# Kernel optimization log

Hardware: AMD Instinct MI355X
Metric: run time of the kernel (lower is better)

## Reference

```python
import jax, jax.numpy as jnp
import numpy as np

B, CIN, COUT, H, W = 8, 256, 256, 64, 64


def setup_inputs() -> dict:
    key = jax.random.key(0)
    k1, k2, k3 = jax.random.split(key, 3)
    x = jax.random.normal(k1, (B, CIN, H, W), dtype=jnp.float32)
    style = jax.random.normal(k2, (B, CIN), dtype=jnp.float32)
    # kaiming_normal_ (fan_in = CIN*3*3, gain = sqrt(2))
    fan_in = CIN * 9
    weight = jax.random.normal(k3, (COUT, CIN, 3, 3), dtype=jnp.float32) * np.sqrt(2.0 / fan_in)
    return {"x": x, "style": style, "weight": weight}


def reference(x, style, weight):
    b, cin, h, w = x.shape
    cout = weight.shape[0]
    # modulate: [B, Cout, Cin, 3, 3]
    mw = style[:, None, :, None, None] * weight[None]
    # demodulate
    sigma = jnp.sqrt(jnp.sum(mw * mw, axis=(2, 3, 4), keepdims=True) + 1e-8)
    dw = mw / sigma
    # per-sample conv via grouped convolution (groups = B)
    x_g = x.reshape(1, b * cin, h, w)
    w_g = dw.reshape(b * cout, cin, 3, 3)
    out = jax.lax.conv_general_dilated(
        x_g, w_g,
        window_strides=(1, 1),
        padding=((1, 1), (1, 1)),
        feature_group_count=b,
        dimension_numbers=("NCHW", "OIHW", "NCHW"),
    )
    return out.reshape(b, cout, h, w)
```

## Files before the change

kernel.cpp:

```cpp
#include <hip/hip_runtime.h>

#define B_ 8
#define CIN_ 256
#define COUT_ 256

typedef short short8_t __attribute__((ext_vector_type(8)));
typedef float float16_t __attribute__((ext_vector_type(16)));

#define DWA_SHORTS   (B_ * 9 * 32 * COUT_ * 8)
#define XPRE_SHORTS  (B_ * 8 * 66 * 66 * 32)

__device__ __forceinline__ unsigned short f2bf(float f) {
    union { float f; unsigned u; } v; v.f = f;
    unsigned u = v.u;
    unsigned r = (u + 0x7fffu + ((u >> 16) & 1u)) >> 16;
    return (unsigned short)r;
}

__global__ __launch_bounds__(256) void k_prep(const float* __restrict__ x,
                                              const float* __restrict__ style,
                                              const float* __restrict__ weight,
                                              unsigned short* __restrict__ xpre,
                                              unsigned short* __restrict__ dwA) {
    __shared__ float wlds[4 * 2304];
    const int bid = blockIdx.x;
    const int t = threadIdx.x;

    if (bid < 4224) {
        const int h_out = bid % 66;
        const int t2 = bid / 66;
        const int cb = t2 & 7, b = t2 >> 3;
        const int h_in = h_out - 1;
        unsigned short* dst_row = xpre + ((size_t)(b * 8 + cb) * 66 + h_out) * 66 * 32;
#pragma unroll
        for (int pass = 0; pass < 2; ++pass) {
            int p = t + pass * 256;
            if (p >= 264) break;
            int w_out = p >> 2, g = p & 3;
            int w_in = w_out - 1;
            short8_t v = (short8_t){0, 0, 0, 0, 0, 0, 0, 0};
            if ((unsigned)h_in < 64u && (unsigned)w_in < 64u) {
                const float* xp =
                    x + (((size_t)(b * CIN_ + cb * 32 + g * 8)) * 64 + h_in) * 64 + w_in;
#pragma unroll
                for (int j = 0; j < 8; ++j) v[j] = (short)f2bf(xp[(size_t)j * 4096]);
            }
            *(short8_t*)(dst_row + (size_t)w_out * 32 + g * 8) = v;
        }
    } else {
        const int co0 = (bid - 4224) * 4;
        const int co_l = t >> 6;
        const int lane = t & 63;
        const int co = co0 + co_l;

        const float* wp = weight + (size_t)co0 * 2304;
#pragma unroll
        for (int k = 0; k < 36; ++k) wlds[t + 256 * k] = wp[t + 256 * k];
        __syncthreads();

        float wv[4][9];
        float ss[4];
#pragma unroll
        for (int k = 0; k < 4; ++k) {
            float a = 0.f;
#pragma unroll
            for (int tap = 0; tap < 9; ++tap) {
                float w = wlds[co_l * 2304 + (lane + 64 * k) * 9 + tap];
                wv[k][tap] = w;
                a += w * w;
            }
            ss[k] = a;
        }
        float sv[8][4];
#pragma unroll
        for (int b = 0; b < 8; ++b)
#pragma unroll
            for (int k = 0; k < 4; ++k) sv[b][k] = style[b * CIN_ + lane + 64 * k];

        float inv[8];
#pragma unroll
        for (int b = 0; b < 8; ++b) {
            float part = 0.f;
#pragma unroll
            for (int k = 0; k < 4; ++k) part += sv[b][k] * sv[b][k] * ss[k];
#pragma unroll
            for (int off = 32; off > 0; off >>= 1) part += __shfl_xor(part, off, 64);
            inv[b] = 1.0f / sqrtf(part + 1e-8f);
        }

        const size_t base = (size_t)co * 8 + (lane & 7) + (size_t)(lane >> 3) * 2048;
#pragma unroll
        for (int b = 0; b < 8; ++b)
#pragma unroll
            for (int tap = 0; tap < 9; ++tap)
#pragma unroll
                for (int k = 0; k < 4; ++k) {
                    size_t addr = ((size_t)(b * 9 + tap) * 32 + k * 8) * 2048 + base;
                    dwA[addr] = f2bf(wv[k][tap] * sv[b][k] * inv[b]);
                }
    }
}

__global__ __launch_bounds__(256, 4) void k_conv(const unsigned short* __restrict__ xpre,
                                                 const unsigned short* __restrict__ dwA,
                                                 float* __restrict__ out) {
    __shared__ __align__(16) unsigned short xs[2][12 * 66 * 8];

    const int row = blockIdx.x;
    const int co_tile = blockIdx.y;
    const int b = blockIdx.z;
    const int tid = threadIdx.x;
    const int lane = tid & 63, wid = tid >> 6;
    const int wave_m = wid >> 1, wave_n = wid & 1;
    const int l32 = lane & 31, kh = lane >> 5;
    const int co_base = co_tile * 128 + wave_m * 64;

    float16_t acc[2];
#pragma unroll
    for (int mi = 0; mi < 2; ++mi)
#pragma unroll
        for (int r = 0; r < 16; ++r) acc[mi][r] = 0.f;

    short8_t st[4];
    auto load_regs = [&](int cb) {
        const unsigned short* s = xpre + (((size_t)(b * 8 + cb) * 66 + row)) * (66 * 32);
#pragma unroll
        for (int it = 0; it < 3; ++it) {
            int c = tid + it * 256;
            int rowg = c / 66;
            int col = c - rowg * 66;
            st[it] = *(const short8_t*)(s + (size_t)((rowg >> 2) * 2112 + col * 32 + (rowg & 3) * 8));
        }
        if (tid < 24) {
            int c = tid + 768;
            int rowg = c / 66;
            int col = c - rowg * 66;
            st[3] = *(const short8_t*)(s + (size_t)((rowg >> 2) * 2112 + col * 32 + (rowg & 3) * 8));
        }
    };
    auto store_lds = [&](int buf) {
        unsigned short* d = xs[buf];
#pragma unroll
        for (int it = 0; it < 3; ++it)
            *(short8_t*)(d + (size_t)(tid + it * 256) * 8) = st[it];
        if (tid < 24) *(short8_t*)(d + (size_t)(tid + 768) * 8) = st[3];
    };

    short8_t abuf[2][4];
    auto loadA = [&](short8_t* dst, int acb, int atap) {
        const unsigned short* base = dwA + ((size_t)(b * 9 + atap) * 32 + acb * 4 + kh) * 2048;
#pragma unroll
        for (int mi = 0; mi < 2; ++mi)
#pragma unroll
            for (int ks = 0; ks < 2; ++ks)
                dst[mi * 2 + ks] =
                    *(const short8_t*)(base + (size_t)ks * 4096 + (co_base + mi * 32 + l32) * 8);
    };

    load_regs(0);
    loadA(abuf[0], 0, 0);

    for (int cb = 0; cb < 8; ++cb) {
        store_lds(cb & 1);
        __syncthreads();
        if (cb < 7) load_regs(cb + 1);

        const unsigned short* xb = xs[cb & 1];
#pragma unroll
        for (int tap = 0; tap < 9; ++tap) {
            const int par = (cb + tap) & 1;
            const int nl = tap + 1;
            const int acb = cb + nl / 9, atap = nl % 9;
            if (acb < 8) loadA(abuf[par ^ 1], acb, atap);

            const int dh = tap / 3, dwc = tap - dh * 3;
            const int col = wave_n * 32 + l32 + dwc;
            short8_t bf[2];
#pragma unroll
            for (int ks = 0; ks < 2; ++ks) {
                int g = ks * 2 + kh;
                bf[ks] = *(const short8_t*)(xb + (size_t)((dh * 4 + g) * 66 + col) * 8);
            }
            const short8_t* ac = abuf[par];
#pragma unroll
            for (int ks = 0; ks < 2; ++ks)
#pragma unroll
                for (int mi = 0; mi < 2; ++mi)
                    acc[mi] = __builtin_amdgcn_mfma_f32_32x32x16_bf16(ac[mi * 2 + ks], bf[ks],
                                                                      acc[mi], 0, 0, 0);
        }
    }

    const int colb = wave_n * 32 + l32;
#pragma unroll
    for (int mi = 0; mi < 2; ++mi)
#pragma unroll
        for (int r = 0; r < 16; ++r) {
            int co = co_base + mi * 32 + (r & 3) + 8 * (r >> 2) + 4 * kh;
            out[(((size_t)b * COUT_ + co) * 64 + row) * 64 + colb] = acc[mi][r];
        }
}

extern "C" void kernel_launch(void* const* d_in, const int* in_sizes, int n_in,
                              void* d_out, int out_size, void* d_ws, size_t ws_size,
                              hipStream_t stream) {
    const float* x = (const float*)d_in[0];
    const float* style = (const float*)d_in[1];
    const float* weight = (const float*)d_in[2];
    float* out = (float*)d_out;

    unsigned short* dwA = (unsigned short*)d_ws;
    unsigned short* xpre = dwA + DWA_SHORTS;

    k_prep<<<dim3(4288), 256, 0, stream>>>(x, style, weight, xpre, dwA);
    k_conv<<<dim3(64, 2, B_), 256, 0, stream>>>(xpre, dwA, out);
}
```

Baseline: 153.5 us.

## Split weight demodulation into separate pack kernel and tile conv over two rows

The prep kernel now only computes per-(batch,cout) demodulation factors with a 16-lane reduction. A new k_wpack kernel writes modulated bf16 weights in contiguous per-(batch, cout-block, cin-block, tap) slabs so the conv kernel's A loads are contiguous. The x pre-layout groups channel sub-blocks per row, and each conv block now covers two output rows with a 2x2 MFMA tile per wave, reusing each A fragment across two column halves, with triple-buffered A prefetch. The aim is less A-operand traffic and more scattered-write coalescing in exchange for an extra launch, higher register pressure (launch bounds 2) and half as many conv blocks.

```diff
diff --git a/kernel.cpp b/kernel.cpp
--- a/kernel.cpp
+++ b/kernel.cpp
@@ -7,8 +7,8 @@
 typedef short short8_t __attribute__((ext_vector_type(8)));
 typedef float float16_t __attribute__((ext_vector_type(16)));
 
-#define DWA_SHORTS   (B_ * 9 * 32 * COUT_ * 8)
-#define XPRE_SHORTS  (B_ * 8 * 66 * 66 * 32)
+#define DWA_SHORTS   (B_ * 2 * 8 * 9 * 4 * 128 * 8)
+#define XPRE_SHORTS  (B_ * 8 * 66 * 4 * 66 * 8)
 
 __device__ __forceinline__ unsigned short f2bf(float f) {
     union { float f; unsigned u; } v; v.f = f;
@@ -21,8 +21,7 @@
                                               const float* __restrict__ style,
                                               const float* __restrict__ weight,
                                               unsigned short* __restrict__ xpre,
-                                              unsigned short* __restrict__ dwA) {
-    __shared__ float wlds[4 * 2304];
+                                              float* __restrict__ invp) {
     const int bid = blockIdx.x;
     const int t = threadIdx.x;
 
@@ -31,12 +30,13 @@
         const int t2 = bid / 66;
         const int cb = t2 & 7, b = t2 >> 3;
         const int h_in = h_out - 1;
-        unsigned short* dst_row = xpre + ((size_t)(b * 8 + cb) * 66 + h_out) * 66 * 32;
+        const int g = t >> 6, lane = t & 63;
+        unsigned short* dst =
+            xpre + (((size_t)(b * 8 + cb) * 66 + h_out) * 4 + g) * (66 * 8);
 #pragma unroll
         for (int pass = 0; pass < 2; ++pass) {
-            int p = t + pass * 256;
-            if (p >= 264) break;
-            int w_out = p >> 2, g = p & 3;
+            int w_out = pass * 64 + lane;
+            if (pass == 1 && lane >= 2) break;
             int w_in = w_out - 1;
             short8_t v = (short8_t){0, 0, 0, 0, 0, 0, 0, 0};
             if ((unsigned)h_in < 64u && (unsigned)w_in < 64u) {
@@ -45,120 +45,119 @@
 #pragma unroll
                 for (int j = 0; j < 8; ++j) v[j] = (short)f2bf(xp[(size_t)j * 4096]);
             }
-            *(short8_t*)(dst_row + (size_t)w_out * 32 + g * 8) = v;
+            *(short8_t*)(dst + (size_t)w_out * 8) = v;
         }
     } else {
-        const int co0 = (bid - 4224) * 4;
-        const int co_l = t >> 6;
-        const int lane = t & 63;
-        const int co = co0 + co_l;
-
-        const float* wp = weight + (size_t)co0 * 2304;
-#pragma unroll
-        for (int k = 0; k < 36; ++k) wlds[t + 256 * k] = wp[t + 256 * k];
-        __syncthreads();
-
-        float wv[4][9];
-        float ss[4];
-#pragma unroll
-        for (int k = 0; k < 4; ++k) {
+        const int co = (bid - 4224) * 16 + (t >> 4);
+        const int sl = t & 15;
+        float part[8];
+#pragma unroll
+        for (int b = 0; b < 8; ++b) part[b] = 0.f;
+        const float* wr = weight + (size_t)co * 2304 + sl * 16 * 9;
+#pragma unroll 4
+        for (int k = 0; k < 16; ++k) {
+            int ci = sl * 16 + k;
             float a = 0.f;
 #pragma unroll
-            for (int tap = 0; tap < 9; ++tap) {
-                float w = wlds[co_l * 2304 + (lane + 64 * k) * 9 + tap];
-                wv[k][tap] = w;
-                a += w * w;
+            for (int tp = 0; tp < 9; ++tp) { float w = wr[k * 9 + tp]; a += w * w; }
+#pragma unroll
+            for (int b = 0; b < 8; ++b) {
+                float s = style[b * CIN_ + ci];
+                part[b] += s * s * a;
             }
-            ss[k] = a;
-        }
-        float sv[8][4];
-#pragma unroll
-        for (int b = 0; b < 8; ++b)
-#pragma unroll
-            for (int k = 0; k < 4; ++k) sv[b][k] = style[b * CIN_ + lane + 64 * k];
-
-        float inv[8];
+        }
 #pragma unroll
         for (int b = 0; b < 8; ++b) {
-            float part = 0.f;
-#pragma unroll
-            for (int k = 0; k < 4; ++k) part += sv[b][k] * sv[b][k] * ss[k];
-#pragma unroll
-            for (int off = 32; off > 0; off >>= 1) part += __shfl_xor(part, off, 64);
-            inv[b] = 1.0f / sqrtf(part + 1e-8f);
-        }
-
-        const size_t base = (size_t)co * 8 + (lane & 7) + (size_t)(lane >> 3) * 2048;
-#pragma unroll
-        for (int b = 0; b < 8; ++b)
-#pragma unroll
-            for (int tap = 0; tap < 9; ++tap)
-#pragma unroll
-                for (int k = 0; k < 4; ++k) {
-                    size_t addr = ((size_t)(b * 9 + tap) * 32 + k * 8) * 2048 + base;
-                    dwA[addr] = f2bf(wv[k][tap] * sv[b][k] * inv[b]);
-                }
+            float p = part[b];
+            p += __shfl_xor(p, 1, 64);
+            p += __shfl_xor(p, 2, 64);
+            p += __shfl_xor(p, 4, 64);
+            p += __shfl_xor(p, 8, 64);
+            if (sl == 0) invp[b * COUT_ + co] = 1.0f / sqrtf(p + 1e-8f);
+        }
     }
 }
 
-__global__ __launch_bounds__(256, 4) void k_conv(const unsigned short* __restrict__ xpre,
+__global__ __launch_bounds__(256) void k_wpack(const float* __restrict__ weight,
+                                               const float* __restrict__ style,
+                                               const float* __restrict__ invp,
+                                               unsigned short* __restrict__ dwA) {
+    const int co_blk = blockIdx.x, cb = blockIdx.y, b = blockIdx.z;
+    const int t = threadIdx.x;
+    unsigned short* slab = dwA + (((size_t)(b * 2 + co_blk) * 8 + cb) * 9) * 4096;
+    const int co = co_blk * 128 + (t & 127);
+    const float iv = invp[b * COUT_ + co];
+    const float* wco = weight + (size_t)co * 2304;
+#pragma unroll
+    for (int i = 0; i < 18; ++i) {
+        int o8 = t + i * 256;
+        int g = (o8 >> 7) & 3;
+        int tap = o8 >> 9;
+        int ci0 = cb * 32 + g * 8;
+        short8_t v;
+#pragma unroll
+        for (int k = 0; k < 8; ++k)
+            v[k] = (short)f2bf(wco[(ci0 + k) * 9 + tap] * style[b * CIN_ + ci0 + k] * iv);
+        *(short8_t*)(slab + (size_t)o8 * 8) = v;
+    }
+}
+
+__global__ __launch_bounds__(256, 2) void k_conv(const unsigned short* __restrict__ xpre,
                                                  const unsigned short* __restrict__ dwA,
                                                  float* __restrict__ out) {
-    __shared__ __align__(16) unsigned short xs[2][12 * 66 * 8];
-
-    const int row = blockIdx.x;
-    const int co_tile = blockIdx.y;
+    __shared__ __align__(16) unsigned short xs[2][4 * 4 * 66 * 8];
+
+    const int rowgrp = blockIdx.x;
+    const int co_blk = blockIdx.y;
     const int b = blockIdx.z;
     const int tid = threadIdx.x;
     const int lane = tid & 63, wid = tid >> 6;
-    const int wave_m = wid >> 1, wave_n = wid & 1;
+    const int wave_m = wid & 1;
+    const int wave_r = wid >> 1;
     const int l32 = lane & 31, kh = lane >> 5;
-    const int co_base = co_tile * 128 + wave_m * 64;
-
-    float16_t acc[2];
+    const int r0 = rowgrp * 2;
+
+    float16_t acc[2][2];
 #pragma unroll
     for (int mi = 0; mi < 2; ++mi)
 #pragma unroll
-        for (int r = 0; r < 16; ++r) acc[mi][r] = 0.f;
-
-    short8_t st[4];
+        for (int nj = 0; nj < 2; ++nj)
+#pragma unroll
+            for (int r = 0; r < 16; ++r) acc[mi][nj][r] = 0.f;
+
+    short8_t st[5];
     auto load_regs = [&](int cb) {
-        const unsigned short* s = xpre + (((size_t)(b * 8 + cb) * 66 + row)) * (66 * 32);
-#pragma unroll
-        for (int it = 0; it < 3; ++it) {
-            int c = tid + it * 256;
-            int rowg = c / 66;
-            int col = c - rowg * 66;
-            st[it] = *(const short8_t*)(s + (size_t)((rowg >> 2) * 2112 + col * 32 + (rowg & 3) * 8));
-        }
-        if (tid < 24) {
-            int c = tid + 768;
-            int rowg = c / 66;
-            int col = c - rowg * 66;
-            st[3] = *(const short8_t*)(s + (size_t)((rowg >> 2) * 2112 + col * 32 + (rowg & 3) * 8));
-        }
+        const unsigned short* s =
+            xpre + ((size_t)(b * 8 + cb) * 66 + r0) * (4 * 66 * 8);
+#pragma unroll
+        for (int it = 0; it < 4; ++it)
+            st[it] = *(const short8_t*)(s + (size_t)(tid + it * 256) * 8);
+        if (tid < 32) st[4] = *(const short8_t*)(s + (size_t)(tid + 1024) * 8);
     };
     auto store_lds = [&](int buf) {
         unsigned short* d = xs[buf];
 #pragma unroll
-        for (int it = 0; it < 3; ++it)
+        for (int it = 0; it < 4; ++it)
             *(short8_t*)(d + (size_t)(tid + it * 256) * 8) = st[it];
-        if (tid < 24) *(short8_t*)(d + (size_t)(tid + 768) * 8) = st[3];
+        if (tid < 32) *(short8_t*)(d + (size_t)(tid + 1024) * 8) = st[4];
     };
 
-    short8_t abuf[2][4];
+    short8_t abuf[3][4];
     auto loadA = [&](short8_t* dst, int acb, int atap) {
-        const unsigned short* base = dwA + ((size_t)(b * 9 + atap) * 32 + acb * 4 + kh) * 2048;
-#pragma unroll
-        for (int mi = 0; mi < 2; ++mi)
-#pragma unroll
-            for (int ks = 0; ks < 2; ++ks)
-                dst[mi * 2 + ks] =
-                    *(const short8_t*)(base + (size_t)ks * 4096 + (co_base + mi * 32 + l32) * 8);
+        const unsigned short* Ab =
+            dwA + ((((size_t)(b * 2 + co_blk) * 8 + acb) * 9 + atap)) * 4096;
+        const int co_off = wave_m * 64 + l32;
+#pragma unroll
+        for (int ks = 0; ks < 2; ++ks)
+#pragma unroll
+            for (int mi = 0; mi < 2; ++mi)
+                dst[ks * 2 + mi] = *(const short8_t*)(
+                    Ab + (size_t)((ks * 2 + kh) * 128 + co_off + mi * 32) * 8);
     };
 
     load_regs(0);
     loadA(abuf[0], 0, 0);
+    loadA(abuf[1], 0, 1);
 
     for (int cb = 0; cb < 8; ++cb) {
         store_lds(cb & 1);
@@ -168,37 +167,43 @@
         const unsigned short* xb = xs[cb & 1];
 #pragma unroll
         for (int tap = 0; tap < 9; ++tap) {
-            const int par = (cb + tap) & 1;
-            const int nl = tap + 1;
+            const int nl = tap + 2;
             const int acb = cb + nl / 9, atap = nl % 9;
-            if (acb < 8) loadA(abuf[par ^ 1], acb, atap);
+            if (acb < 8) loadA(abuf[(tap + 2) % 3], acb, atap);
 
             const int dh = tap / 3, dwc = tap - dh * 3;
-            const int col = wave_n * 32 + l32 + dwc;
-            short8_t bf[2];
-#pragma unroll
-            for (int ks = 0; ks < 2; ++ks) {
-                int g = ks * 2 + kh;
-                bf[ks] = *(const short8_t*)(xb + (size_t)((dh * 4 + g) * 66 + col) * 8);
+            const unsigned short* bb =
+                xb + (size_t)(((wave_r + dh) * 4 + kh) * 66 + l32 + dwc) * 8;
+            short8_t bf[2][2];
+#pragma unroll
+            for (int ks = 0; ks < 2; ++ks)
+#pragma unroll
+                for (int nj = 0; nj < 2; ++nj)
+                    bf[ks][nj] = *(const short8_t*)(bb + (size_t)(ks * 2 * 66 + nj * 32) * 8);
+
+            const short8_t* ac = abuf[tap % 3];
+#pragma unroll
+            for (int ks = 0; ks < 2; ++ks)
+#pragma unroll
+                for (int mi = 0; mi < 2; ++mi)
+#pragma unroll
+                    for (int nj = 0; nj < 2; ++nj)
+                        acc[mi][nj] = __builtin_amdgcn_mfma_f32_32x32x16_bf16(
+                            ac[ks * 2 + mi], bf[ks][nj], acc[mi][nj], 0, 0, 0);
+        }
+    }
+
+    const int orow = r0 + wave_r;
+#pragma unroll
+    for (int mi = 0; mi < 2; ++mi)
+#pragma unroll
+        for (int nj = 0; nj < 2; ++nj)
+#pragma unroll
+            for (int r = 0; r < 16; ++r) {
+                int co = co_blk * 128 + wave_m * 64 + mi * 32 + (r & 3) + 8 * (r >> 2) + 4 * kh;
+                int c = nj * 32 + l32;
+                out[(((size_t)b * COUT_ + co) * 64 + orow) * 64 + c] = acc[mi][nj][r];
             }
-            const short8_t* ac = abuf[par];
-#pragma unroll
-            for (int ks = 0; ks < 2; ++ks)
-#pragma unroll
-                for (int mi = 0; mi < 2; ++mi)
-                    acc[mi] = __builtin_amdgcn_mfma_f32_32x32x16_bf16(ac[mi * 2 + ks], bf[ks],
-                                                                      acc[mi], 0, 0, 0);
-        }
-    }
-
-    const int colb = wave_n * 32 + l32;
-#pragma unroll
-    for (int mi = 0; mi < 2; ++mi)
-#pragma unroll
-        for (int r = 0; r < 16; ++r) {
-            int co = co_base + mi * 32 + (r & 3) + 8 * (r >> 2) + 4 * kh;
-            out[(((size_t)b * COUT_ + co) * 64 + row) * 64 + colb] = acc[mi][r];
-        }
 }
 
 extern "C" void kernel_launch(void* const* d_in, const int* in_sizes, int n_in,
@@ -211,7 +216,9 @@
 
     unsigned short* dwA = (unsigned short*)d_ws;
     unsigned short* xpre = dwA + DWA_SHORTS;
-
-    k_prep<<<dim3(4288), 256, 0, stream>>>(x, style, weight, xpre, dwA);
-    k_conv<<<dim3(64, 2, B_), 256, 0, stream>>>(xpre, dwA, out);
-}
+    float* invp = (float*)(xpre + XPRE_SHORTS);
+
+    k_prep<<<dim3(4240), 256, 0, stream>>>(x, style, weight, xpre, invp);
+    k_wpack<<<dim3(2, 8, B_), 256, 0, stream>>>(weight, style, invp, dwA);
+    k_conv<<<dim3(32, 2, B_), 256, 0, stream>>>(xpre, dwA, out);
+}
```

Result: no change. 152.8 us (-0.4%).
